# Optimization experiments

Hardware: AMD Instinct MI355X
Metric: run time of the kernel (lower is better)

## Reference

```python
import jax, jax.numpy as jnp
import numpy as np

KERNEL_SIZE = 5
SIGMA = 1.0
DARK_KS = 15


def _gaussian_kernel():
    x = jnp.arange(KERNEL_SIZE, dtype=jnp.float32) - KERNEL_SIZE // 2
    phi = jnp.exp(-0.5 * x * x / (SIGMA ** 2))
    phi = phi / (phi.sum() + 0.001)
    k2d = jnp.outer(phi, phi)                       # [5,5]
    return jnp.tile(k2d[None, None], (3, 1, 1, 1))  # [3,1,5,5] OIHW depthwise


def _tanh01(v):
    return jnp.tanh(v) * 0.5 + 0.5


def setup_inputs() -> dict:
    key = jax.random.key(0)
    k1, k2, k3 = jax.random.split(key, 3)
    # keep x strictly positive so x**param has well-defined gradients
    x = jax.random.uniform(k1, (16, 3, 512, 512), dtype=jnp.float32, minval=0.01, maxval=1.0)
    output1 = jax.random.normal(k2, (16, 7), dtype=jnp.float32)
    output2 = jax.random.normal(k3, (16, 4), dtype=jnp.float32)
    return {"x": x, "output1": output1, "output2": output2}


def reference(x, output1, output2):
    N, C, H, W = x.shape

    # ---- parameter squashing (clip_range + softmax weights) ----
    o1 = jnp.concatenate([
        _tanh01(output1[:, 0:1]) * 0.25 + 1.0,   # gamma param in [1, 1.25]
        _tanh01(output1[:, 1:2]) * 0.9 + 0.1,    # contrast alpha (dead branch)
        _tanh01(output1[:, 2:3]) * 2.0,          # sharpen lamda in [0, 2]
        _tanh01(output1[:, 3:4]),                # dehaze w in [0, 1]
        _tanh01(output1[:, 4:7]) * 0.1 + 0.95,   # WB gains in [0.95, 1.05]
    ], axis=1)
    o2 = jax.nn.softmax(_tanh01(output2), axis=1)  # [N,4] branch weights

    param = o1[:, 0][:, None, None, None]
    lamda = o1[:, 2][:, None, None, None]
    w = o1[:, 3][:, None, None, None]
    wb_params = o1[:, 4:7][:, :, None, None]

    # ---- WB ----
    x1 = jnp.clip(x * wb_params, 0.0, 1.0)

    # ---- GAMMA ----
    x2 = jnp.clip(x ** param + 0.001, 0.0, 1.0)

    # ---- SHARPEN (depthwise 5x5 gaussian blur, unsharp mask) ----
    gk = _gaussian_kernel()
    blur = jax.lax.conv_general_dilated(
        x, gk, window_strides=(1, 1), padding=((2, 2), (2, 2)),
        feature_group_count=3,
        dimension_numbers=("NCHW", "OIHW", "NCHW"))
    blur = jnp.clip(blur, 0.0, 1.0)
    x4 = jnp.clip(x + lamda * (x - blur), 0.0, 1.0)

    # ---- DEHAZE ----
    minc = jnp.min(x, axis=1, keepdims=True)  # [N,1,H,W]
    # avg_pool2d k=15 s=1 p=7 with count_include_pad=True -> sum window / 225
    dark = jax.lax.reduce_window(
        minc, 0.0, jax.lax.add, (1, 1, DARK_KS, DARK_KS), (1, 1, 1, 1),
        padding=[(0, 0), (0, 0), (DARK_KS // 2, DARK_KS // 2), (DARK_KS // 2, DARK_KS // 2)]
    ) / float(DARK_KS * DARK_KS)
    top_k = int(H * W * 0.05)
    flat_dark = dark.reshape(N, -1)
    _, top_idx = jax.lax.top_k(flat_dark, top_k)            # [N, top_k]
    flat_img = x.reshape(N, C, -1)
    sel = jnp.take_along_axis(flat_img, top_idx[:, None, :], axis=2)  # [N,C,top_k]
    A = sel.mean(axis=2)[:, :, None, None]                  # atmospheric light
    trans = 1.0 - w * dark
    trans = jnp.where(trans > 0.1, trans, jnp.float32(0.1))
    x5 = jnp.clip((x - A) / (trans + 0.001) + A, 0.0, 1.0)

    # ---- weighted combination (contrast branch is computed but unused upstream) ----
    w0 = o2[:, 0][:, None, None, None]
    w1 = o2[:, 1][:, None, None, None]
    w2 = o2[:, 2][:, None, None, None]
    w3 = o2[:, 3][:, None, None, None]
    x_sum = x + 0.1 * (w0 * x1 + w1 * x2 + w2 * x4 + w3 * x5)
    x_sum = x_sum / (jnp.sum(o2, axis=1)[:, None, None, None] + 0.001)

    # ---- per-sample per-channel min-max normalization ----
    min_vals = jnp.min(x_sum, axis=(2, 3), keepdims=True)
    max_vals = jnp.max(x_sum, axis=(2, 3), keepdims=True)
    return (x_sum - min_vals) / (max_vals - min_vals + 1e-07)
```

## Files before the change

### kernel.cpp

```cpp
#include <hip/hip_runtime.h>
#include <math.h>

#define NS   16
#define HH   512
#define WW   512
#define HW   (HH*WW)
#define TOPK 13107
#define NBIN 1024

#define O_O1   0
#define O_O2   112
#define O_DEN  176
#define O_KN   304
#define O_MMP  512
#define O_PART 25088
#define O_DARK 33280


#define G0 0.054466787f
#define G1 0.244103071f
#define G2 0.402457854f

__device__ __forceinline__ float tanh01(float v) { return tanhf(v)*0.5f + 0.5f; }
__device__ __forceinline__ float clamp01(float v) { return fminf(fmaxf(v, 0.0f), 1.0f); }
__device__ __forceinline__ int dark_bin(float v) {
  int b = (int)(v * (float)NBIN);
  return b > (NBIN-1) ? (NBIN-1) : (b < 0 ? 0 : b);
}

__global__ void k_zero(unsigned* __restrict__ hist, float* __restrict__ wsf,
                       const float* __restrict__ o1, const float* __restrict__ o2) {
  int i = blockIdx.x * 256 + threadIdx.x;
  uint4 z; z.x = 0u; z.y = 0u; z.z = 0u; z.w = 0u;
  ((uint4*)hist)[i] = z;
  if (threadIdx.x == 0) {
    int n = blockIdx.x;
    wsf[O_O1+n*7+0] = tanh01(o1[n*7+0])*0.25f + 1.0f;
    wsf[O_O1+n*7+1] = tanh01(o1[n*7+1])*0.9f  + 0.1f;
    wsf[O_O1+n*7+2] = tanh01(o1[n*7+2])*2.0f;
    wsf[O_O1+n*7+3] = tanh01(o1[n*7+3]);
    wsf[O_O1+n*7+4] = tanh01(o1[n*7+4])*0.1f + 0.95f;
    wsf[O_O1+n*7+5] = tanh01(o1[n*7+5])*0.1f + 0.95f;
    wsf[O_O1+n*7+6] = tanh01(o1[n*7+6])*0.1f + 0.95f;
    float q0 = expf(tanh01(o2[n*4+0]));
    float q1 = expf(tanh01(o2[n*4+1]));
    float q2 = expf(tanh01(o2[n*4+2]));
    float q3 = expf(tanh01(o2[n*4+3]));
    float s = q0+q1+q2+q3;
    q0 /= s; q1 /= s; q2 /= s; q3 /= s;
    wsf[O_O2+n*4+0]=q0; wsf[O_O2+n*4+1]=q1; wsf[O_O2+n*4+2]=q2; wsf[O_O2+n*4+3]=q3;
    wsf[O_DEN+n] = (q0+q1+q2+q3) + 0.001f;
  }
}

__global__ void __launch_bounds__(512)
k_dark(const float* __restrict__ x, float* __restrict__ wsf, unsigned* __restrict__ hist) {
  __shared__ __align__(16) float sm[6240 + 78*64];
  float* minc = sm;
  unsigned* lh = (unsigned*)sm;
  float* hsum = sm + 6240;
  int tid = threadIdx.x;
  int w0 = blockIdx.x * 64, h0 = blockIdx.y * 64, n = blockIdx.z;
  const float* xb = x + (size_t)n*3*HW;

  bool interior = (w0 >= 8) && (w0 + 72 <= WW) && (h0 >= 7) && (h0 + 71 <= HH);
  if (interior) {
    for (int i = tid; i < 78*20; i += 512) {
      int r = i / 20, q = i - r*20;
      size_t o = (size_t)(h0 - 7 + r)*WW + (w0 - 8 + 4*q);
      float4 a = *(const float4*)&xb[o];
      float4 b = *(const float4*)&xb[HW + o];
      float4 c = *(const float4*)&xb[2*HW + o];
      float4 v;
      v.x = fminf(fminf(a.x,b.x),c.x); v.y = fminf(fminf(a.y,b.y),c.y);
      v.z = fminf(fminf(a.z,b.z),c.z); v.w = fminf(fminf(a.w,b.w),c.w);
      *(float4*)&minc[r*80 + 4*q] = v;
    }
  } else {
    for (int i = tid; i < 78*20; i += 512) {
      int r = i / 20, q = i - r*20;
      int hm = h0 - 7 + r, wc = w0 - 8 + 4*q;
      float4 v; v.x = 0.f; v.y = 0.f; v.z = 0.f; v.w = 0.f;
      if (hm >= 0 && hm < HH && wc >= 0 && wc < WW) {
        size_t o = (size_t)hm*WW + wc;
        float4 a = *(const float4*)&xb[o];
        float4 b = *(const float4*)&xb[HW + o];
        float4 c = *(const float4*)&xb[2*HW + o];
        v.x = fminf(fminf(a.x,b.x),c.x); v.y = fminf(fminf(a.y,b.y),c.y);
        v.z = fminf(fminf(a.z,b.z),c.z); v.w = fminf(fminf(a.w,b.w),c.w);
      }
      *(float4*)&minc[r*80 + 4*q] = v;
    }
  }
  __syncthreads();
  for (int i = tid; i < 78*16; i += 512) {
    int r = i >> 4, c4 = (i & 15) * 4;
    const float4* mr = (const float4*)&minc[r*80];
    int qb = c4 >> 2;
    float m[20];
    #pragma unroll
    for (int t = 0; t < 5; ++t) {
      float4 v = mr[qb + t];
      m[4*t] = v.x; m[4*t+1] = v.y; m[4*t+2] = v.z; m[4*t+3] = v.w;
    }
    float s = 0.f;
    #pragma unroll
    for (int j = 1; j <= 15; ++j) s += m[j];
    float4 o;
    o.x = s; s += m[16] - m[1];
    o.y = s; s += m[17] - m[2];
    o.z = s; s += m[18] - m[3];
    o.w = s;
    *(float4*)&hsum[r*64 + c4] = o;
  }
  __syncthreads();
  for (int i = tid; i < NBIN*4; i += 512) lh[i] = 0u;
  __syncthreads();
  {
    int c = tid & 63, ty = tid >> 6, r0 = ty * 8;
    int rep = tid & 3;
    float s = 0.f;
    #pragma unroll
    for (int j = 0; j < 15; ++j) s += hsum[(r0 + j)*64 + c];
    float* dk = wsf + O_DARK + (size_t)n*HW;
    int prevb = -1; unsigned cnt = 0;
    #pragma unroll
    for (int i = 0; i < 8; ++i) {
      int r = r0 + i;
      float v = s * (1.0f/225.0f);
      dk[(size_t)(h0 + r)*WW + w0 + c] = v;
      int b = dark_bin(v);
      if (b == prevb) { cnt++; }
      else {
        if (cnt) atomicAdd(&lh[(prevb << 2) | rep], cnt);
        prevb = b; cnt = 1u;
      }
      if (i < 7) s += hsum[(r + 15)*64 + c] - hsum[r*64 + c];
    }
    atomicAdd(&lh[(prevb << 2) | rep], cnt);
  }
  __syncthreads();
  unsigned* gh = hist + n*NBIN;
  for (int b = tid; b < NBIN; b += 512) {
    unsigned v = lh[4*b] + lh[4*b+1] + lh[4*b+2] + lh[4*b+3];
    if (v) atomicAdd(&gh[b], v);
  }
}

__global__ void __launch_bounds__(256)
k_asum(const float* __restrict__ x, float* __restrict__ wsf,
       const unsigned* __restrict__ hist, unsigned* __restrict__ wsu) {
  __shared__ __align__(16) unsigned lh[NBIN];
  __shared__ unsigned spp[256];
  __shared__ unsigned wtot[4];
  __shared__ int sh_bsel;
  __shared__ unsigned sh_kn;
  __shared__ float bl[4][7];
  int tid = threadIdx.x;
  int lane = tid & 63, wave = tid >> 6;
  int n = blockIdx.x >> 6, chunk = blockIdx.x & 63;
  {
    uint4 v = ((const uint4*)(hist + n*NBIN))[tid];
    *(uint4*)&lh[tid*4] = v;
    spp[tid] = v.x + v.y + v.z + v.w;
  }
  __syncthreads();
  unsigned sv = spp[tid];
  #pragma unroll
  for (int off = 1; off < 64; off <<= 1) {
    unsigned u = __shfl_down(sv, off);
    if (lane + off < 64) sv += u;
  }
  if (lane == 0) wtot[wave] = sv;
  __syncthreads();
  unsigned above = 0;
  #pragma unroll
  for (int w2 = 1; w2 < 4; ++w2) above += (wave + w2 < 4) ? wtot[wave + w2] : 0u;
  unsigned S = sv + above;
  unsigned Snext = S - spp[tid];
  if (S >= (unsigned)TOPK && Snext < (unsigned)TOPK) {
    unsigned cum = Snext;
    int bsel = tid*4;
    for (int b = tid*4 + 3; b >= tid*4; --b) {
      if (cum + lh[b] >= (unsigned)TOPK) { bsel = b; break; }
      cum += lh[b];
    }
    sh_bsel = bsel;
    sh_kn = (unsigned)TOPK - cum;
  }
  __syncthreads();
  int bsel = sh_bsel;
  if (tid == 0 && chunk == 0) wsu[O_KN + n] = sh_kn;
  const float4* db = (const float4*)(wsf + O_DARK + (size_t)n*HW + (size_t)chunk*4096);
  const float4* x0 = (const float4*)(x + (size_t)n*3*HW + (size_t)chunk*4096);
  const float4* x1 = x0 + HW/4;
  const float4* x2 = x0 + HW/2;
  float s0=0,s1=0,s2=0,e0=0,e1=0,e2=0,ec=0;
  #pragma unroll
  for (int k = 0; k < 4; ++k) {
    int idx = k*256 + tid;
    float4 d = db[idx];
    int bbx = dark_bin(d.x), bby = dark_bin(d.y);
    int bbz = dark_bin(d.z), bbw = dark_bin(d.w);
    int bmax = bbx > bby ? bbx : bby;
    bmax = bbz > bmax ? bbz : bmax;
    bmax = bbw > bmax ? bbw : bmax;
    if (bmax >= bsel) {
      float4 a = x0[idx], b = x1[idx], c = x2[idx];
      #define ACC(BB, AX, BX, CX) { \
        bool gt = (BB > bsel), eq = (BB == bsel); \
        s0 += gt ? AX : 0.f; s1 += gt ? BX : 0.f; s2 += gt ? CX : 0.f; \
        e0 += eq ? AX : 0.f; e1 += eq ? BX : 0.f; e2 += eq ? CX : 0.f; \
        ec += eq ? 1.f : 0.f; }
      ACC(bbx, a.x, b.x, c.x) ACC(bby, a.y, b.y, c.y)
      ACC(bbz, a.z, b.z, c.z) ACC(bbw, a.w, b.w, c.w)
      #undef ACC
    }
  }
  #pragma unroll
  for (int off = 32; off; off >>= 1) {
    s0 += __shfl_down(s0, off); s1 += __shfl_down(s1, off); s2 += __shfl_down(s2, off);
    e0 += __shfl_down(e0, off); e1 += __shfl_down(e1, off); e2 += __shfl_down(e2, off);
    ec += __shfl_down(ec, off);
  }
  if (lane == 0) {
    bl[wave][0]=s0; bl[wave][1]=s1; bl[wave][2]=s2;
    bl[wave][3]=e0; bl[wave][4]=e1; bl[wave][5]=e2; bl[wave][6]=ec;
  }
  __syncthreads();
  if (tid < 7) wsf[O_PART + blockIdx.x*8 + tid] =
      bl[0][tid] + bl[1][tid] + bl[2][tid] + bl[3][tid];
}

__global__ void __launch_bounds__(256)
k_main(const float* __restrict__ x, float* __restrict__ wsf,
       const unsigned* __restrict__ wsu, float* __restrict__ out) {
  __shared__ __align__(16) float xs[36*72];
  __shared__ __align__(16) float hb[36*68];
  __shared__ float rmn[4], rmx[4];
  __shared__ float shA[3];
  int tid = threadIdx.x;
  int w0 = blockIdx.x * 64, h0 = blockIdx.y * 32, n = blockIdx.z;
  int r2 = tid >> 4, c4 = (tid & 15) * 4;
  int wave = tid >> 6, lane = tid & 63;
  int bxy = blockIdx.y * 8 + blockIdx.x;
  const float* dkp = wsf + O_DARK + (size_t)n*HW + (size_t)(h0 + 2*r2)*WW + w0 + c4;
  float4 dk0 = *(const float4*)dkp;
  float4 dk1 = *(const float4*)(dkp + WW);
  float param = wsf[O_O1 + n*7 + 0];
  float lamda = wsf[O_O1 + n*7 + 2];
  float wpar  = wsf[O_O1 + n*7 + 3];
  float q0 = wsf[O_O2 + n*4 + 0], q1 = wsf[O_O2 + n*4 + 1];
  float q2 = wsf[O_O2 + n*4 + 2], q3 = wsf[O_O2 + n*4 + 3];
  float rden = 1.0f / wsf[O_DEN + n];
  bool interior = (w0 >= 4) && (w0 + 68 <= WW) && (h0 >= 2) && (h0 + 34 <= HH);
  if (tid < 64) {
    const float* p = wsf + O_PART + (size_t)(n*64 + tid)*8;
    float s0=p[0], s1=p[1], s2=p[2], e0=p[3], e1=p[4], e2=p[5], ec=p[6];
    #pragma unroll
    for (int off = 32; off; off >>= 1) {
      s0 += __shfl_down(s0, off); s1 += __shfl_down(s1, off); s2 += __shfl_down(s2, off);
      e0 += __shfl_down(e0, off); e1 += __shfl_down(e1, off); e2 += __shfl_down(e2, off);
      ec += __shfl_down(ec, off);
    }
    if (tid == 0) {
      float kn = (float)wsu[O_KN + n];
      float ce = fmaxf(ec, 1.0f);
      shA[0] = (s0 + kn * (e0 / ce)) * (1.0f/(float)TOPK);
      shA[1] = (s1 + kn * (e1 / ce)) * (1.0f/(float)TOPK);
      shA[2] = (s2 + kn * (e2 / ce)) * (1.0f/(float)TOPK);
    }
  }

  for (int c = 0; c < 3; ++c) {
    int z = n*3 + c;
    const float* xc = x + (size_t)z*HW;
    if (interior) {
      for (int i = tid; i < 648; i += 256) {
        int rr = i / 18, q = i - rr*18;
        *(float4*)&xs[rr*72 + 4*q] =
            *(const float4*)&xc[(size_t)(h0 - 2 + rr)*WW + (w0 - 4 + 4*q)];
      }
    } else {
      for (int i = tid; i < 648; i += 256) {
        int rr = i / 18, q = i - rr*18;
        int gh = h0 - 2 + rr, gw = w0 - 4 + 4*q;
        float4 v; v.x = 0.f; v.y = 0.f; v.z = 0.f; v.w = 0.f;
        if (gh >= 0 && gh < HH && gw >= 0 && gw < WW)
          v = *(const float4*)&xc[(size_t)gh*WW + gw];
        *(float4*)&xs[rr*72 + 4*q] = v;
      }
    }
    __syncthreads();
    for (int i = tid; i < 576; i += 256) {
      int rr = i >> 4, cc4 = (i & 15) * 4;
      const float4* xr = (const float4*)&xs[rr*72];
      int qb = cc4 >> 2;
      float4 A4 = xr[qb], B4 = xr[qb+1], C4 = xr[qb+2];
      float m2=A4.z, m3=A4.w, m4=B4.x, m5=B4.y, m6=B4.z, m7=B4.w, m8=C4.x, m9=C4.y;
      float4 o;
      o.x = G0*(m2+m6) + G1*(m3+m5) + G2*m4;
      o.y = G0*(m3+m7) + G1*(m4+m6) + G2*m5;
      o.z = G0*(m4+m8) + G1*(m5+m7) + G2*m6;
      o.w = G0*(m5+m9) + G1*(m6+m8) + G2*m7;
      *(float4*)&hb[rr*68 + cc4] = o;
    }
    __syncthreads();
    float wb = wsf[O_O1 + n*7 + 4 + c];
    float A  = shA[c];
    float4 xv0 = *(const float4*)&xs[(2*r2+2)*72 + c4 + 4];
    float4 xv1 = *(const float4*)&xs[(2*r2+3)*72 + c4 + 4];
    float4 b0 = *(const float4*)&hb[(2*r2+0)*68 + c4];
    float4 b1 = *(const float4*)&hb[(2*r2+1)*68 + c4];
    float4 b2 = *(const float4*)&hb[(2*r2+2)*68 + c4];
    float4 b3 = *(const float4*)&hb[(2*r2+3)*68 + c4];
    float4 b4 = *(const float4*)&hb[(2*r2+4)*68 + c4];
    float4 b5 = *(const float4*)&hb[(2*r2+5)*68 + c4];
    float4 os0, os1;
    float mnv = 3.4e38f, mxv = -3.4e38f;
    #define PIX(OX, XV, B0, B1, B2, B3, B4, DK) { \
      float blur = clamp01(G0*(B0+B4) + G1*(B1+B3) + G2*B2); \
      float x4v = clamp01(XV + lamda*(XV - blur)); \
      float x1v = clamp01(XV * wb); \
      float x2v = clamp01(__expf(param*__logf(XV)) + 0.001f); \
      float tr = 1.0f - wpar*DK; tr = tr > 0.1f ? tr : 0.1f; \
      float x5v = clamp01((XV - A) * __builtin_amdgcn_rcpf(tr + 0.001f) + A); \
      OX = (XV + 0.1f*(q0*x1v + q1*x2v + q2*x4v + q3*x5v)) * rden; \
      mnv = fminf(mnv, OX); mxv = fmaxf(mxv, OX); }
    PIX(os0.x, xv0.x, b0.x, b1.x, b2.x, b3.x, b4.x, dk0.x)
    PIX(os0.y, xv0.y, b0.y, b1.y, b2.y, b3.y, b4.y, dk0.y)
    PIX(os0.z, xv0.z, b0.z, b1.z, b2.z, b3.z, b4.z, dk0.z)
    PIX(os0.w, xv0.w, b0.w, b1.w, b2.w, b3.w, b4.w, dk0.w)
    PIX(os1.x, xv1.x, b1.x, b2.x, b3.x, b4.x, b5.x, dk1.x)
    PIX(os1.y, xv1.y, b1.y, b2.y, b3.y, b4.y, b5.y, dk1.y)
    PIX(os1.z, xv1.z, b1.z, b2.z, b3.z, b4.z, b5.z, dk1.z)
    PIX(os1.w, xv1.w, b1.w, b2.w, b3.w, b4.w, b5.w, dk1.w)
    #undef PIX
    float* op = out + (size_t)z*HW + (size_t)(h0 + 2*r2)*WW + w0 + c4;
    *(float4*)op = os0;
    *(float4*)(op + WW) = os1;
    #pragma unroll
    for (int off = 32; off; off >>= 1) {
      mnv = fminf(mnv, __shfl_down(mnv, off));
      mxv = fmaxf(mxv, __shfl_down(mxv, off));
    }
    if (lane == 0) { rmn[wave] = mnv; rmx[wave] = mxv; }
    __syncthreads();
    if (tid == 0) {
      mnv = fminf(fminf(rmn[0], rmn[1]), fminf(rmn[2], rmn[3]));
      mxv = fmaxf(fmaxf(rmx[0], rmx[1]), fmaxf(rmx[2], rmx[3]));
      wsf[O_MMP + z*512 + bxy]       = mnv;
      wsf[O_MMP + z*512 + 256 + bxy] = mxv;
    }
  }
}

__global__ void __launch_bounds__(256)
k_norm(float* __restrict__ out, const float* __restrict__ wsf) {
  __shared__ float rmn[4], rmx[4];
  int tid = threadIdx.x;
  int nc = blockIdx.x >> 5;
  int sub = blockIdx.x & 31;
  float mn = (tid < 128) ? wsf[O_MMP + nc*512 + tid]       :  3.4e38f;
  float mx = (tid < 128) ? wsf[O_MMP + nc*512 + 256 + tid] : -3.4e38f;
  #pragma unroll
  for (int off = 32; off; off >>= 1) {
    mn = fminf(mn, __shfl_down(mn, off));
    mx = fmaxf(mx, __shfl_down(mx, off));
  }
  int wave = tid >> 6, lane = tid & 63;
  if (lane == 0) { rmn[wave] = mn; rmx[wave] = mx; }
  __syncthreads();
  mn = fminf(fminf(rmn[0], rmn[1]), fminf(rmn[2], rmn[3]));
  mx = fmaxf(fmaxf(rmx[0], rmx[1]), fmaxf(rmx[2], rmx[3]));
  float sc = 1.0f / (mx - mn + 1e-7f);
  float4* o4 = (float4*)out + (size_t)nc*65536 + (size_t)sub*2048;
  #pragma unroll
  for (int k = 0; k < 8; ++k) {
    float4 v = o4[k*256 + tid];
    v.x = (v.x - mn) * sc; v.y = (v.y - mn) * sc;
    v.z = (v.z - mn) * sc; v.w = (v.w - mn) * sc;
    o4[k*256 + tid] = v;
  }
}

extern "C" void kernel_launch(void* const* d_in, const int* in_sizes, int n_in,
                              void* d_out, int out_size, void* d_ws, size_t ws_size,
                              hipStream_t stream) {
  const float* x  = (const float*)d_in[0];
  const float* o1 = (const float*)d_in[1];
  const float* o2 = (const float*)d_in[2];
  float* out = (float*)d_out;
  float* wsf = (float*)d_ws;
  unsigned* wsu = (unsigned*)d_ws;
  unsigned* hist = (unsigned*)(out + (size_t)16*HW);

  k_zero<<<dim3(16), dim3(256), 0, stream>>>(hist, wsf, o1, o2);
  k_dark<<<dim3(8, 8, 16), dim3(512), 0, stream>>>(x, wsf, hist);
  k_asum<<<dim3(1024), dim3(256), 0, stream>>>(x, wsf, hist, wsu);
  k_main<<<dim3(8, 16, 16), dim3(256), 0, stream>>>(x, wsf, wsu, out);
  k_norm<<<dim3(1536), dim3(256), 0, stream>>>(out, wsf);
}
```

Before: 165.4 us.

## Fold parameter setup into k_dark, memset histogram, halve asum grid, simplify norm reduce

Removes the k_zero kernel: the histogram is cleared with hipMemsetAsync and the parameter squashing moves into the first block of each sample in k_dark. k_asum now uses 32 chunks per sample with 8 float4 iterations per thread, and k_main reduces only 32 partials. k_main preloads the white-balance gains into registers, and k_norm replaces its cross-wave shared-memory reduction with a single-wave shuffle and broadcast. The goal is to cut one launch and some small-kernel overhead, at the cost of less parallelism in k_asum.

```diff
diff --git a/kernel.cpp b/kernel.cpp
--- a/kernel.cpp
+++ b/kernel.cpp
@@ -28,13 +28,18 @@
   return b > (NBIN-1) ? (NBIN-1) : (b < 0 ? 0 : b);
 }
 
-__global__ void k_zero(unsigned* __restrict__ hist, float* __restrict__ wsf,
-                       const float* __restrict__ o1, const float* __restrict__ o2) {
-  int i = blockIdx.x * 256 + threadIdx.x;
-  uint4 z; z.x = 0u; z.y = 0u; z.z = 0u; z.w = 0u;
-  ((uint4*)hist)[i] = z;
-  if (threadIdx.x == 0) {
-    int n = blockIdx.x;
+__global__ void __launch_bounds__(512)
+k_dark(const float* __restrict__ x, float* __restrict__ wsf, unsigned* __restrict__ hist,
+       const float* __restrict__ o1, const float* __restrict__ o2) {
+  __shared__ __align__(16) float sm[6240 + 78*64];
+  float* minc = sm;
+  unsigned* lh = (unsigned*)sm;
+  float* hsum = sm + 6240;
+  int tid = threadIdx.x;
+  int w0 = blockIdx.x * 64, h0 = blockIdx.y * 64, n = blockIdx.z;
+  const float* xb = x + (size_t)n*3*HW;
+
+  if (blockIdx.x == 0 && blockIdx.y == 0 && tid == 0) {
     wsf[O_O1+n*7+0] = tanh01(o1[n*7+0])*0.25f + 1.0f;
     wsf[O_O1+n*7+1] = tanh01(o1[n*7+1])*0.9f  + 0.1f;
     wsf[O_O1+n*7+2] = tanh01(o1[n*7+2])*2.0f;
@@ -51,17 +56,6 @@
     wsf[O_O2+n*4+0]=q0; wsf[O_O2+n*4+1]=q1; wsf[O_O2+n*4+2]=q2; wsf[O_O2+n*4+3]=q3;
     wsf[O_DEN+n] = (q0+q1+q2+q3) + 0.001f;
   }
-}
-
-__global__ void __launch_bounds__(512)
-k_dark(const float* __restrict__ x, float* __restrict__ wsf, unsigned* __restrict__ hist) {
-  __shared__ __align__(16) float sm[6240 + 78*64];
-  float* minc = sm;
-  unsigned* lh = (unsigned*)sm;
-  float* hsum = sm + 6240;
-  int tid = threadIdx.x;
-  int w0 = blockIdx.x * 64, h0 = blockIdx.y * 64, n = blockIdx.z;
-  const float* xb = x + (size_t)n*3*HW;
 
   bool interior = (w0 >= 8) && (w0 + 72 <= WW) && (h0 >= 7) && (h0 + 71 <= HH);
   if (interior) {
@@ -158,7 +152,7 @@
   __shared__ float bl[4][7];
   int tid = threadIdx.x;
   int lane = tid & 63, wave = tid >> 6;
-  int n = blockIdx.x >> 6, chunk = blockIdx.x & 63;
+  int n = blockIdx.x >> 5, chunk = blockIdx.x & 31;
   {
     uint4 v = ((const uint4*)(hist + n*NBIN))[tid];
     *(uint4*)&lh[tid*4] = v;
@@ -191,13 +185,13 @@
   __syncthreads();
   int bsel = sh_bsel;
   if (tid == 0 && chunk == 0) wsu[O_KN + n] = sh_kn;
-  const float4* db = (const float4*)(wsf + O_DARK + (size_t)n*HW + (size_t)chunk*4096);
-  const float4* x0 = (const float4*)(x + (size_t)n*3*HW + (size_t)chunk*4096);
+  const float4* db = (const float4*)(wsf + O_DARK + (size_t)n*HW) + (size_t)chunk*2048;
+  const float4* x0 = (const float4*)(x + (size_t)n*3*HW) + (size_t)chunk*2048;
   const float4* x1 = x0 + HW/4;
   const float4* x2 = x0 + HW/2;
   float s0=0,s1=0,s2=0,e0=0,e1=0,e2=0,ec=0;
   #pragma unroll
-  for (int k = 0; k < 4; ++k) {
+  for (int k = 0; k < 8; ++k) {
     int idx = k*256 + tid;
     float4 d = db[idx];
     int bbx = dark_bin(d.x), bby = dark_bin(d.y);
@@ -250,13 +244,20 @@
   float param = wsf[O_O1 + n*7 + 0];
   float lamda = wsf[O_O1 + n*7 + 2];
   float wpar  = wsf[O_O1 + n*7 + 3];
+  float wbc[3];
+  wbc[0] = wsf[O_O1 + n*7 + 4];
+  wbc[1] = wsf[O_O1 + n*7 + 5];
+  wbc[2] = wsf[O_O1 + n*7 + 6];
   float q0 = wsf[O_O2 + n*4 + 0], q1 = wsf[O_O2 + n*4 + 1];
   float q2 = wsf[O_O2 + n*4 + 2], q3 = wsf[O_O2 + n*4 + 3];
   float rden = 1.0f / wsf[O_DEN + n];
   bool interior = (w0 >= 4) && (w0 + 68 <= WW) && (h0 >= 2) && (h0 + 34 <= HH);
   if (tid < 64) {
-    const float* p = wsf + O_PART + (size_t)(n*64 + tid)*8;
-    float s0=p[0], s1=p[1], s2=p[2], e0=p[3], e1=p[4], e2=p[5], ec=p[6];
+    float s0=0,s1=0,s2=0,e0=0,e1=0,e2=0,ec=0;
+    if (tid < 32) {
+      const float* p = wsf + O_PART + (size_t)(n*32 + tid)*8;
+      s0=p[0]; s1=p[1]; s2=p[2]; e0=p[3]; e1=p[4]; e2=p[5]; ec=p[6];
+    }
     #pragma unroll
     for (int off = 32; off; off >>= 1) {
       s0 += __shfl_down(s0, off); s1 += __shfl_down(s1, off); s2 += __shfl_down(s2, off);
@@ -306,7 +307,7 @@
       *(float4*)&hb[rr*68 + cc4] = o;
     }
     __syncthreads();
-    float wb = wsf[O_O1 + n*7 + 4 + c];
+    float wb = wbc[c];
     float A  = shA[c];
     float4 xv0 = *(const float4*)&xs[(2*r2+2)*72 + c4 + 4];
     float4 xv1 = *(const float4*)&xs[(2*r2+3)*72 + c4 + 4];
@@ -357,22 +358,20 @@
 
 __global__ void __launch_bounds__(256)
 k_norm(float* __restrict__ out, const float* __restrict__ wsf) {
-  __shared__ float rmn[4], rmx[4];
   int tid = threadIdx.x;
   int nc = blockIdx.x >> 5;
   int sub = blockIdx.x & 31;
-  float mn = (tid < 128) ? wsf[O_MMP + nc*512 + tid]       :  3.4e38f;
-  float mx = (tid < 128) ? wsf[O_MMP + nc*512 + 256 + tid] : -3.4e38f;
+  int l = tid & 63;
+  const float* pm = wsf + O_MMP + (size_t)nc*512;
+  float mn = fminf(pm[l], pm[64 + l]);
+  float mx = fmaxf(pm[256 + l], pm[320 + l]);
   #pragma unroll
   for (int off = 32; off; off >>= 1) {
     mn = fminf(mn, __shfl_down(mn, off));
     mx = fmaxf(mx, __shfl_down(mx, off));
   }
-  int wave = tid >> 6, lane = tid & 63;
-  if (lane == 0) { rmn[wave] = mn; rmx[wave] = mx; }
-  __syncthreads();
-  mn = fminf(fminf(rmn[0], rmn[1]), fminf(rmn[2], rmn[3]));
-  mx = fmaxf(fmaxf(rmx[0], rmx[1]), fmaxf(rmx[2], rmx[3]));
+  mn = __shfl(mn, 0);
+  mx = __shfl(mx, 0);
   float sc = 1.0f / (mx - mn + 1e-7f);
   float4* o4 = (float4*)out + (size_t)nc*65536 + (size_t)sub*2048;
   #pragma unroll
@@ -395,9 +394,9 @@
   unsigned* wsu = (unsigned*)d_ws;
   unsigned* hist = (unsigned*)(out + (size_t)16*HW);
 
-  k_zero<<<dim3(16), dim3(256), 0, stream>>>(hist, wsf, o1, o2);
-  k_dark<<<dim3(8, 8, 16), dim3(512), 0, stream>>>(x, wsf, hist);
-  k_asum<<<dim3(1024), dim3(256), 0, stream>>>(x, wsf, hist, wsu);
+  hipMemsetAsync(hist, 0, (size_t)NS*NBIN*sizeof(unsigned), stream);
+  k_dark<<<dim3(8, 8, 16), dim3(512), 0, stream>>>(x, wsf, hist, o1, o2);
+  k_asum<<<dim3(512), dim3(256), 0, stream>>>(x, wsf, hist, wsu);
   k_main<<<dim3(8, 16, 16), dim3(256), 0, stream>>>(x, wsf, wsu, out);
   k_norm<<<dim3(1536), dim3(256), 0, stream>>>(out, wsf);
 }
```

Result: faster. 161.9 us (-2.1%).
